# Kernel tuning notes

Measured on AMD Instinct MI355X. Metric: run time of the kernel, lower is better.

Reference implementation:

```python
import jax, jax.numpy as jnp
import numpy as np

N = 262144          # num keyframes
E = 1048576         # num visual links (edges)
DT = 0.1            # IMU integration step
L1, L2, L3, L4 = 1.0, 0.5, 2.0, 0.5
EPS = 1e-6

# ---- quaternion helpers (pypose convention: q = [x, y, z, w]) ----

def qmul(q1, q2):
    v1, w1 = q1[..., :3], q1[..., 3:4]
    v2, w2 = q2[..., :3], q2[..., 3:4]
    w = w1 * w2 - jnp.sum(v1 * v2, axis=-1, keepdims=True)
    v = w1 * v2 + w2 * v1 + jnp.cross(v1, v2)
    return jnp.concatenate([v, w], axis=-1)

def qconj(q):
    return jnp.concatenate([-q[..., :3], q[..., 3:4]], axis=-1)

def qrot(q, x):
    # rotate vector x by unit quaternion q: x + 2*cross(v, cross(v,x) + w*x)
    v, w = q[..., :3], q[..., 3:4]
    return x + 2.0 * jnp.cross(v, jnp.cross(v, x) + w * x)

def so3_log(q):
    # log map of unit quaternion -> axis-angle phi (..., 3)
    v, w = q[..., :3], q[..., 3:4]
    n = jnp.linalg.norm(v, axis=-1, keepdims=True)
    n_safe = jnp.where(n < EPS, 1.0, n)
    theta = 2.0 * jnp.arctan2(n, w)
    w_safe = jnp.where(jnp.abs(w) < EPS, 1.0, w)
    factor = jnp.where(n < EPS, 2.0 / w_safe, theta / n_safe)
    return factor * v

def se3_inv(p):
    t, q = p[..., :3], p[..., 3:]
    qi = qconj(q)
    ti = -qrot(qi, t)
    return jnp.concatenate([ti, qi], axis=-1)

def se3_mul(p1, p2):
    t1, q1 = p1[..., :3], p1[..., 3:]
    t2, q2 = p2[..., :3], p2[..., 3:]
    t = t1 + qrot(q1, t2)
    return jnp.concatenate([t, qmul(q1, q2)], axis=-1)

def se3_log(p):
    # returns se(3) tensor [tau, phi] (pypose order) with tau = Jl^{-1}(phi) t
    t, q = p[..., :3], p[..., 3:]
    phi = so3_log(q)
    th = jnp.linalg.norm(phi, axis=-1, keepdims=True)
    th_safe = jnp.where(th < EPS, 1.0, th)
    coef = jnp.where(
        th < EPS,
        1.0 / 12.0 + th * th / 720.0,
        1.0 / (th_safe * th_safe)
        - (1.0 + jnp.cos(th_safe)) / (2.0 * th_safe * jnp.sin(th_safe)),
    )
    pxt = jnp.cross(phi, t)
    tau = t - 0.5 * pxt + coef * jnp.cross(phi, pxt)
    return jnp.concatenate([tau, phi], axis=-1)


def setup_inputs() -> dict:
    key = jax.random.key(0)
    ks = jax.random.split(key, 8)

    def unit_quat(k, n):
        q = jax.random.normal(k, (n, 4), dtype=jnp.float32)
        return q / jnp.linalg.norm(q, axis=-1, keepdims=True)

    pose = jnp.concatenate(
        [jax.random.normal(ks[0], (N, 3), dtype=jnp.float32),
         unit_quat(ks[1], N)], axis=-1)
    vel = jax.random.normal(ks[2], (N, 3), dtype=jnp.float32)
    vmot = jnp.concatenate(
        [0.1 * jax.random.normal(ks[3], (E, 3), dtype=jnp.float32),
         unit_quat(ks[4], E)], axis=-1)
    imu_drot = unit_quat(ks[5], N - 1)
    body_dvel = 0.1 * jax.random.normal(ks[6], (N - 1, 3), dtype=jnp.float32)
    body_dpos = 0.1 * jax.random.normal(ks[7], (N - 1, 3), dtype=jnp.float32)
    vlink = jax.random.randint(jax.random.fold_in(key, 99), (E, 2), 0, N)
    return dict(pose=pose, vel=vel, vmot=vmot, imu_drot=imu_drot,
                body_dvel=body_dvel, body_dpos=body_dpos, vlink=vlink)


def reference(pose, vel, vmot, imu_drot, body_dvel, body_dpos, vlink):
    trans, rot = pose[:, :3], pose[:, 3:]
    r1 = rot[:-1]

    # IMU model: world-frame increments (rotation-dependent, as in original)
    imu_dvel = qrot(r1, body_dvel)                      # world_dvel(pose.rotation())
    imu_dpos = qrot(r1, body_dpos) + vel[:-1] * DT      # world_dpos(rot, vel)

    # pose-graph residual: Log(vmot^{-1} @ pose1^{-1} @ pose2)  [E, 6]
    pose1 = pose[vlink[:, 0]]
    pose2 = pose[vlink[:, 1]]
    err = se3_mul(se3_inv(vmot), se3_mul(se3_inv(pose1), pose2))
    pgerr = se3_log(err)

    # adjacent velocity residual [N-1, 3]
    adjvelerr = imu_dvel - jnp.diff(vel, axis=0)

    # IMU rotation residual: Log(imu_drot @ R1^{-1} @ R2)  [N-1, 3]
    q_rel = qmul(imu_drot, qmul(qconj(rot[:-1]), rot[1:]))
    imuroterr = so3_log(q_rel)

    # translation/velocity residual [N-1, 3]
    transvelerr = imu_dpos - jnp.diff(trans, axis=0)

    return jnp.concatenate([
        L1 * pgerr.reshape(-1),
        L2 * adjvelerr.reshape(-1),
        L3 * imuroterr.reshape(-1),
        L4 * transvelerr.reshape(-1),
    ], axis=0)
```

## Files before the change

kernel.cpp:

```cpp
#include <hip/hip_runtime.h>
#include <math.h>

constexpr int   NN  = 262144;
constexpr int   NE  = 1048576;
constexpr int   NE2 = NE / 2;
constexpr float DTc = 0.1f;
constexpr float W1 = 1.0f, W2 = 0.5f, W3 = 2.0f, W4 = 0.5f;
constexpr float EPSc = 1e-6f;

typedef float    __attribute__((ext_vector_type(2))) f32x2;
typedef float    __attribute__((ext_vector_type(4))) f32x4;
typedef float    __attribute__((ext_vector_type(4), aligned(4))) f32x4u;
typedef float    __attribute__((ext_vector_type(2), aligned(4))) f32x2u;
typedef int      __attribute__((ext_vector_type(2))) i32x2;
typedef _Float16 __attribute__((ext_vector_type(8))) f16x8;

struct V3 { float x, y, z; };
struct Q4 { float x, y, z, w; };

__device__ __forceinline__ V3 v3(float x, float y, float z) { V3 r{x, y, z}; return r; }
__device__ __forceinline__ V3 vadd(V3 a, V3 b) { return v3(a.x + b.x, a.y + b.y, a.z + b.z); }
__device__ __forceinline__ V3 vsub(V3 a, V3 b) { return v3(a.x - b.x, a.y - b.y, a.z - b.z); }
__device__ __forceinline__ V3 vscale(float s, V3 a) { return v3(s * a.x, s * a.y, s * a.z); }
__device__ __forceinline__ V3 vcross(V3 a, V3 b) {
    return v3(a.y * b.z - a.z * b.y, a.z * b.x - a.x * b.z, a.x * b.y - a.y * b.x);
}
__device__ __forceinline__ float vdot(V3 a, V3 b) { return a.x * b.x + a.y * b.y + a.z * b.z; }

__device__ __forceinline__ Q4 qmul(Q4 a, Q4 b) {
    Q4 r;
    r.w = a.w * b.w - (a.x * b.x + a.y * b.y + a.z * b.z);
    r.x = a.w * b.x + b.w * a.x + (a.y * b.z - a.z * b.y);
    r.y = a.w * b.y + b.w * a.y + (a.z * b.x - a.x * b.z);
    r.z = a.w * b.z + b.w * a.z + (a.x * b.y - a.y * b.x);
    return r;
}
__device__ __forceinline__ Q4 qconj(Q4 q) { Q4 r{-q.x, -q.y, -q.z, q.w}; return r; }
__device__ __forceinline__ V3 qrot(Q4 q, V3 x) {
    V3 v = v3(q.x, q.y, q.z);
    V3 c1 = vadd(vcross(v, x), vscale(q.w, x));
    return vadd(x, vscale(2.0f, vcross(v, c1)));
}
__device__ __forceinline__ V3 so3_log(Q4 q) {
    V3 v = v3(q.x, q.y, q.z);
    float n = sqrtf(vdot(v, v));
    float theta = 2.0f * atan2f(n, q.w);
    float factor;
    if (n < EPSc) {
        float w_safe = (fabsf(q.w) < EPSc) ? 1.0f : q.w;
        factor = 2.0f / w_safe;
    } else {
        factor = theta / n;
    }
    return vscale(factor, v);
}

__device__ __forceinline__ void edge_residual(V3 tm, Q4 qm, V3 t1, Q4 q1,
                                              V3 t2, Q4 q2, float* __restrict__ o) {
    Q4 qa = qconj(q1);
    V3 ta = vscale(-1.0f, qrot(qa, t1));
    V3 tb = vadd(ta, qrot(qa, t2));
    Q4 qb = qmul(qa, q2);
    Q4 qc = qconj(qm);
    V3 tc = vscale(-1.0f, qrot(qc, tm));
    V3 te = vadd(tc, qrot(qc, tb));
    Q4 qe = qmul(qc, qb);

    V3 phi = so3_log(qe);
    float th = sqrtf(vdot(phi, phi));
    float coef;
    if (th < EPSc) {
        coef = 1.0f / 12.0f + th * th / 720.0f;
    } else {
        float s, c;
        sincosf(th, &s, &c);
        coef = 1.0f / (th * th) - (1.0f + c) / (2.0f * th * s);
    }
    V3 pxt = vcross(phi, te);
    V3 tau = vadd(vsub(te, vscale(0.5f, pxt)), vscale(coef, vcross(phi, pxt)));

    f32x2* o2 = (f32x2*)o;
    f32x2 a = {W1 * tau.x, W1 * tau.y};
    f32x2 b = {W1 * tau.z, W1 * phi.x};
    f32x2 c = {W1 * phi.y, W1 * phi.z};
    __builtin_nontemporal_store(a, o2);
    __builtin_nontemporal_store(b, o2 + 1);
    __builtin_nontemporal_store(c, o2 + 2);
}

__global__ __launch_bounds__(256) void node_pack_kernel(
    const float* __restrict__ pose, const float* __restrict__ vel,
    const float* __restrict__ imu_drot, const float* __restrict__ body_dvel,
    const float* __restrict__ body_dpos, f16x8* __restrict__ ppH,
    float* __restrict__ out)
{
    int i = blockIdx.x * blockDim.x + threadIdx.x;
    if (i >= NN) return;
    f32x4u pa0 = *(const f32x4u*)(pose + 7 * (size_t)i);
    f32x4u pa1 = *(const f32x4u*)(pose + 7 * (size_t)i + 3);
    f16x8 rec = {(_Float16)pa0.x, (_Float16)pa0.y, (_Float16)pa0.z,
                 (_Float16)pa1.x, (_Float16)pa1.y, (_Float16)pa1.z,
                 (_Float16)pa1.w, (_Float16)0.0f};
    ppH[i] = rec;
    if (i >= NN - 1) return;

    V3 tr1 = v3(pa0.x, pa0.y, pa0.z); Q4 r1 = {pa1.x, pa1.y, pa1.z, pa1.w};
    f32x4u pb0 = *(const f32x4u*)(pose + 7 * (size_t)(i + 1));
    f32x4u pb1 = *(const f32x4u*)(pose + 7 * (size_t)(i + 1) + 3);
    V3 tr2 = v3(pb0.x, pb0.y, pb0.z); Q4 r2 = {pb1.x, pb1.y, pb1.z, pb1.w};

    f32x4u vv = *(const f32x4u*)(vel + 3 * (size_t)i);
    f32x2u vw = *(const f32x2u*)(vel + 3 * (size_t)i + 4);
    V3 v1 = v3(vv.x, vv.y, vv.z);
    V3 v2 = v3(vv.w, vw.x, vw.y);
    f32x2u bv0 = *(const f32x2u*)(body_dvel + 3 * (size_t)i);
    float  bv2 = body_dvel[3 * (size_t)i + 2];
    f32x2u bp0 = *(const f32x2u*)(body_dpos + 3 * (size_t)i);
    float  bp2 = body_dpos[3 * (size_t)i + 2];
    V3 bdv = v3(bv0.x, bv0.y, bv2);
    V3 bdp = v3(bp0.x, bp0.y, bp2);
    f32x4 id4 = *(const f32x4*)(imu_drot + 4 * (size_t)i);
    Q4 idr = {id4.x, id4.y, id4.z, id4.w};

    V3 imu_dvel = qrot(r1, bdv);
    V3 adjvel = vsub(imu_dvel, vsub(v2, v1));
    Q4 qrel = qmul(idr, qmul(qconj(r1), r2));
    V3 imurot = so3_log(qrel);
    V3 imu_dpos = vadd(qrot(r1, bdp), vscale(DTc, v1));
    V3 transvel = vsub(imu_dpos, vsub(tr2, tr1));

    size_t base = (size_t)6 * NE;
    size_t nm1 = (size_t)(NN - 1);
    float* oa = out + base + 3 * (size_t)i;
    oa[0] = W2 * adjvel.x; oa[1] = W2 * adjvel.y; oa[2] = W2 * adjvel.z;
    float* ob = out + base + 3 * nm1 + 3 * (size_t)i;
    ob[0] = W3 * imurot.x; ob[1] = W3 * imurot.y; ob[2] = W3 * imurot.z;
    float* oc = out + base + 6 * nm1 + 3 * (size_t)i;
    oc[0] = W4 * transvel.x; oc[1] = W4 * transvel.y; oc[2] = W4 * transvel.z;
}

__global__ __launch_bounds__(256) void edge_kernel(
    const float* __restrict__ vmot, const int* __restrict__ vlink,
    const f16x8* __restrict__ ppH, float* __restrict__ out)
{
    int tid = blockIdx.x * blockDim.x + threadIdx.x;
    if (tid >= NE2) return;
    int e0 = tid, e1 = tid + NE2;

    i32x2 l0 = __builtin_nontemporal_load((const i32x2*)vlink + e0);
    i32x2 l1 = __builtin_nontemporal_load((const i32x2*)vlink + e1);
    f32x4u m0a = __builtin_nontemporal_load((const f32x4u*)(vmot + 7 * (size_t)e0));
    f32x4u m0b = __builtin_nontemporal_load((const f32x4u*)(vmot + 7 * (size_t)e0 + 3));
    f32x4u m1a = __builtin_nontemporal_load((const f32x4u*)(vmot + 7 * (size_t)e1));
    f32x4u m1b = __builtin_nontemporal_load((const f32x4u*)(vmot + 7 * (size_t)e1 + 3));
    f16x8 g10 = ppH[l0.x];
    f16x8 g20 = ppH[l0.y];
    f16x8 g11 = ppH[l1.x];
    f16x8 g21 = ppH[l1.y];

    edge_residual(v3(m0a.x, m0a.y, m0a.z), Q4{m0b.x, m0b.y, m0b.z, m0b.w},
                  v3((float)g10[0], (float)g10[1], (float)g10[2]),
                  Q4{(float)g10[3], (float)g10[4], (float)g10[5], (float)g10[6]},
                  v3((float)g20[0], (float)g20[1], (float)g20[2]),
                  Q4{(float)g20[3], (float)g20[4], (float)g20[5], (float)g20[6]},
                  out + 6 * (size_t)e0);
    edge_residual(v3(m1a.x, m1a.y, m1a.z), Q4{m1b.x, m1b.y, m1b.z, m1b.w},
                  v3((float)g11[0], (float)g11[1], (float)g11[2]),
                  Q4{(float)g11[3], (float)g11[4], (float)g11[5], (float)g11[6]},
                  v3((float)g21[0], (float)g21[1], (float)g21[2]),
                  Q4{(float)g21[3], (float)g21[4], (float)g21[5], (float)g21[6]},
                  out + 6 * (size_t)e1);
}

__global__ __launch_bounds__(256) void vigraph_fallback(
    const float* __restrict__ pose, const float* __restrict__ vel,
    const float* __restrict__ vmot, const float* __restrict__ imu_drot,
    const float* __restrict__ body_dvel, const float* __restrict__ body_dpos,
    const int* __restrict__ vlink, float* __restrict__ out)
{
    int tid = blockIdx.x * blockDim.x + threadIdx.x;
    if (tid < NE) {
        int e = tid;
        const float* pm = vmot + 7 * (size_t)e;
        int i1 = vlink[2 * (size_t)e];
        int i2 = vlink[2 * (size_t)e + 1];
        const float* p1 = pose + 7 * (size_t)i1;
        const float* p2 = pose + 7 * (size_t)i2;
        edge_residual(v3(pm[0], pm[1], pm[2]), Q4{pm[3], pm[4], pm[5], pm[6]},
                      v3(p1[0], p1[1], p1[2]), Q4{p1[3], p1[4], p1[5], p1[6]},
                      v3(p2[0], p2[1], p2[2]), Q4{p2[3], p2[4], p2[5], p2[6]},
                      out + 6 * (size_t)e);
    } else {
        int i = tid - NE;
        if (i >= NN - 1) return;
        const float* pa = pose + 7 * (size_t)i;
        const float* pb = pose + 7 * (size_t)(i + 1);
        V3 tr1 = v3(pa[0], pa[1], pa[2]); Q4 r1 = {pa[3], pa[4], pa[5], pa[6]};
        V3 tr2 = v3(pb[0], pb[1], pb[2]); Q4 r2 = {pb[3], pb[4], pb[5], pb[6]};
        V3 v1 = v3(vel[3 * (size_t)i], vel[3 * (size_t)i + 1], vel[3 * (size_t)i + 2]);
        V3 v2 = v3(vel[3 * (size_t)(i + 1)], vel[3 * (size_t)(i + 1) + 1], vel[3 * (size_t)(i + 1) + 2]);
        V3 bdv = v3(body_dvel[3 * (size_t)i], body_dvel[3 * (size_t)i + 1], body_dvel[3 * (size_t)i + 2]);
        V3 bdp = v3(body_dpos[3 * (size_t)i], body_dpos[3 * (size_t)i + 1], body_dpos[3 * (size_t)i + 2]);
        Q4 idr = {imu_drot[4 * (size_t)i], imu_drot[4 * (size_t)i + 1],
                  imu_drot[4 * (size_t)i + 2], imu_drot[4 * (size_t)i + 3]};
        V3 imu_dvel = qrot(r1, bdv);
        V3 adjvel = vsub(imu_dvel, vsub(v2, v1));
        Q4 qrel = qmul(idr, qmul(qconj(r1), r2));
        V3 imurot = so3_log(qrel);
        V3 imu_dpos = vadd(qrot(r1, bdp), vscale(DTc, v1));
        V3 transvel = vsub(imu_dpos, vsub(tr2, tr1));
        size_t base = (size_t)6 * NE;
        size_t nm1 = (size_t)(NN - 1);
        float* oa = out + base + 3 * (size_t)i;
        oa[0] = W2 * adjvel.x; oa[1] = W2 * adjvel.y; oa[2] = W2 * adjvel.z;
        float* ob = out + base + 3 * nm1 + 3 * (size_t)i;
        ob[0] = W3 * imurot.x; ob[1] = W3 * imurot.y; ob[2] = W3 * imurot.z;
        float* oc = out + base + 6 * nm1 + 3 * (size_t)i;
        oc[0] = W4 * transvel.x; oc[1] = W4 * transvel.y; oc[2] = W4 * transvel.z;
    }
}

extern "C" void kernel_launch(void* const* d_in, const int* in_sizes, int n_in,
                              void* d_out, int out_size, void* d_ws, size_t ws_size,
                              hipStream_t stream) {
    const float* pose      = (const float*)d_in[0];
    const float* vel       = (const float*)d_in[1];
    const float* vmot      = (const float*)d_in[2];
    const float* imu_drot  = (const float*)d_in[3];
    const float* body_dvel = (const float*)d_in[4];
    const float* body_dpos = (const float*)d_in[5];
    const int*   vlink     = (const int*)d_in[6];
    float* out = (float*)d_out;

    const size_t table_bytes = (size_t)NN * 16;
    if (ws_size >= table_bytes) {
        f16x8* ppH = (f16x8*)d_ws;
        node_pack_kernel<<<NN / 256, 256, 0, stream>>>(pose, vel, imu_drot,
                                                       body_dvel, body_dpos, ppH, out);
        edge_kernel<<<NE2 / 256, 256, 0, stream>>>(vmot, vlink, ppH, out);
    } else {
        int total = NE + (NN - 1);
        int grid = (total + 255) / 256;
        vigraph_fallback<<<grid, 256, 0, stream>>>(pose, vel, vmot, imu_drot,
                                                   body_dvel, body_dpos, vlink, out);
    }
}
```

Measured before the change: 40.23 us.

## Process adjacent edge pairs per thread with wide loads and split node kernel

Each edge thread now handles two consecutive edges instead of edges e and e+NE/2, so vlink is read as one 16-byte load, vmot as contiguous 56 bytes, and the 12 outputs go out as three 16-byte nontemporal stores. The node pack is split into a light pack kernel that runs before the edge kernel, and the IMU residual work moves to a separate kernel launched after it. The SE3 algebra is also simplified to rotate t2-t1 and tb-tm once each instead of rotating twice. The split adds a third kernel launch and puts the pose read in two separate kernels.

New measurement: 42.73 us. 1.06x slower.

```diff
diff --git a/kernel.cpp b/kernel.cpp
--- a/kernel.cpp
+++ b/kernel.cpp
@@ -3,7 +3,7 @@
 
 constexpr int   NN  = 262144;
 constexpr int   NE  = 1048576;
-constexpr int   NE2 = NE / 2;
+constexpr int   NEP = NE / 2;
 constexpr float DTc = 0.1f;
 constexpr float W1 = 1.0f, W2 = 0.5f, W3 = 2.0f, W4 = 0.5f;
 constexpr float EPSc = 1e-6f;
@@ -12,7 +12,7 @@
 typedef float    __attribute__((ext_vector_type(4))) f32x4;
 typedef float    __attribute__((ext_vector_type(4), aligned(4))) f32x4u;
 typedef float    __attribute__((ext_vector_type(2), aligned(4))) f32x2u;
-typedef int      __attribute__((ext_vector_type(2))) i32x2;
+typedef int      __attribute__((ext_vector_type(4))) i32x4;
 typedef _Float16 __attribute__((ext_vector_type(8))) f16x8;
 
 struct V3 { float x, y, z; };
@@ -55,15 +55,15 @@
     return vscale(factor, v);
 }
 
-__device__ __forceinline__ void edge_residual(V3 tm, Q4 qm, V3 t1, Q4 q1,
-                                              V3 t2, Q4 q2, float* __restrict__ o) {
+struct TP { V3 tau; V3 phi; };
+
+__device__ __forceinline__ TP edge_residual(V3 tm, Q4 qm, V3 t1, Q4 q1,
+                                            V3 t2, Q4 q2) {
     Q4 qa = qconj(q1);
-    V3 ta = vscale(-1.0f, qrot(qa, t1));
-    V3 tb = vadd(ta, qrot(qa, t2));
+    V3 tb = qrot(qa, vsub(t2, t1));
     Q4 qb = qmul(qa, q2);
     Q4 qc = qconj(qm);
-    V3 tc = vscale(-1.0f, qrot(qc, tm));
-    V3 te = vadd(tc, qrot(qc, tb));
+    V3 te = qrot(qc, vsub(tb, tm));
     Q4 qe = qmul(qc, qb);
 
     V3 phi = so3_log(qe);
@@ -78,32 +78,70 @@
     }
     V3 pxt = vcross(phi, te);
     V3 tau = vadd(vsub(te, vscale(0.5f, pxt)), vscale(coef, vcross(phi, pxt)));
-
-    f32x2* o2 = (f32x2*)o;
-    f32x2 a = {W1 * tau.x, W1 * tau.y};
-    f32x2 b = {W1 * tau.z, W1 * phi.x};
-    f32x2 c = {W1 * phi.y, W1 * phi.z};
-    __builtin_nontemporal_store(a, o2);
-    __builtin_nontemporal_store(b, o2 + 1);
-    __builtin_nontemporal_store(c, o2 + 2);
-}
-
-__global__ __launch_bounds__(256) void node_pack_kernel(
+    TP r; r.tau = tau; r.phi = phi; return r;
+}
+
+__global__ __launch_bounds__(256) void pack_kernel(const float* __restrict__ pose,
+                                                   f16x8* __restrict__ ppH) {
+    int i = blockIdx.x * blockDim.x + threadIdx.x;
+    if (i >= NN) return;
+    f32x4u a = *(const f32x4u*)(pose + 7 * (size_t)i);
+    f32x4u b = *(const f32x4u*)(pose + 7 * (size_t)i + 3);
+    f16x8 rec = {(_Float16)a.x, (_Float16)a.y, (_Float16)a.z,
+                 (_Float16)b.x, (_Float16)b.y, (_Float16)b.z,
+                 (_Float16)b.w, (_Float16)0.0f};
+    ppH[i] = rec;
+}
+
+__global__ __launch_bounds__(256) void edge_kernel(
+    const float* __restrict__ vmot, const int* __restrict__ vlink,
+    const f16x8* __restrict__ ppH, float* __restrict__ out)
+{
+    int t = blockIdx.x * blockDim.x + threadIdx.x;
+    if (t >= NEP) return;
+
+    i32x4 l = __builtin_nontemporal_load((const i32x4*)vlink + t);
+    f16x8 g10 = ppH[l.x];
+    f16x8 g20 = ppH[l.y];
+    f16x8 g11 = ppH[l.z];
+    f16x8 g21 = ppH[l.w];
+    const float* pm = vmot + 14 * (size_t)t;
+    f32x4u ma = *(const f32x4u*)(pm);
+    f32x4u mb = *(const f32x4u*)(pm + 4);
+    f32x4u mc = *(const f32x4u*)(pm + 8);
+    f32x2u md = *(const f32x2u*)(pm + 12);
+
+    TP r0 = edge_residual(
+        v3(ma.x, ma.y, ma.z), Q4{ma.w, mb.x, mb.y, mb.z},
+        v3((float)g10[0], (float)g10[1], (float)g10[2]),
+        Q4{(float)g10[3], (float)g10[4], (float)g10[5], (float)g10[6]},
+        v3((float)g20[0], (float)g20[1], (float)g20[2]),
+        Q4{(float)g20[3], (float)g20[4], (float)g20[5], (float)g20[6]});
+    TP r1 = edge_residual(
+        v3(mb.w, mc.x, mc.y), Q4{mc.z, mc.w, md.x, md.y},
+        v3((float)g11[0], (float)g11[1], (float)g11[2]),
+        Q4{(float)g11[3], (float)g11[4], (float)g11[5], (float)g11[6]},
+        v3((float)g21[0], (float)g21[1], (float)g21[2]),
+        Q4{(float)g21[3], (float)g21[4], (float)g21[5], (float)g21[6]});
+
+    f32x4* o4 = (f32x4*)(out + 12 * (size_t)t);
+    f32x4 s0 = {W1 * r0.tau.x, W1 * r0.tau.y, W1 * r0.tau.z, W1 * r0.phi.x};
+    f32x4 s1 = {W1 * r0.phi.y, W1 * r0.phi.z, W1 * r1.tau.x, W1 * r1.tau.y};
+    f32x4 s2 = {W1 * r1.tau.z, W1 * r1.phi.x, W1 * r1.phi.y, W1 * r1.phi.z};
+    __builtin_nontemporal_store(s0, o4);
+    __builtin_nontemporal_store(s1, o4 + 1);
+    __builtin_nontemporal_store(s2, o4 + 2);
+}
+
+__global__ __launch_bounds__(256) void node_kernel(
     const float* __restrict__ pose, const float* __restrict__ vel,
     const float* __restrict__ imu_drot, const float* __restrict__ body_dvel,
-    const float* __restrict__ body_dpos, f16x8* __restrict__ ppH,
-    float* __restrict__ out)
+    const float* __restrict__ body_dpos, float* __restrict__ out)
 {
     int i = blockIdx.x * blockDim.x + threadIdx.x;
-    if (i >= NN) return;
+    if (i >= NN - 1) return;
     f32x4u pa0 = *(const f32x4u*)(pose + 7 * (size_t)i);
     f32x4u pa1 = *(const f32x4u*)(pose + 7 * (size_t)i + 3);
-    f16x8 rec = {(_Float16)pa0.x, (_Float16)pa0.y, (_Float16)pa0.z,
-                 (_Float16)pa1.x, (_Float16)pa1.y, (_Float16)pa1.z,
-                 (_Float16)pa1.w, (_Float16)0.0f};
-    ppH[i] = rec;
-    if (i >= NN - 1) return;
-
     V3 tr1 = v3(pa0.x, pa0.y, pa0.z); Q4 r1 = {pa1.x, pa1.y, pa1.z, pa1.w};
     f32x4u pb0 = *(const f32x4u*)(pose + 7 * (size_t)(i + 1));
     f32x4u pb1 = *(const f32x4u*)(pose + 7 * (size_t)(i + 1) + 3);
@@ -137,39 +175,6 @@
     ob[0] = W3 * imurot.x; ob[1] = W3 * imurot.y; ob[2] = W3 * imurot.z;
     float* oc = out + base + 6 * nm1 + 3 * (size_t)i;
     oc[0] = W4 * transvel.x; oc[1] = W4 * transvel.y; oc[2] = W4 * transvel.z;
-}
-
-__global__ __launch_bounds__(256) void edge_kernel(
-    const float* __restrict__ vmot, const int* __restrict__ vlink,
-    const f16x8* __restrict__ ppH, float* __restrict__ out)
-{
-    int tid = blockIdx.x * blockDim.x + threadIdx.x;
-    if (tid >= NE2) return;
-    int e0 = tid, e1 = tid + NE2;
-
-    i32x2 l0 = __builtin_nontemporal_load((const i32x2*)vlink + e0);
-    i32x2 l1 = __builtin_nontemporal_load((const i32x2*)vlink + e1);
-    f32x4u m0a = __builtin_nontemporal_load((const f32x4u*)(vmot + 7 * (size_t)e0));
-    f32x4u m0b = __builtin_nontemporal_load((const f32x4u*)(vmot + 7 * (size_t)e0 + 3));
-    f32x4u m1a = __builtin_nontemporal_load((const f32x4u*)(vmot + 7 * (size_t)e1));
-    f32x4u m1b = __builtin_nontemporal_load((const f32x4u*)(vmot + 7 * (size_t)e1 + 3));
-    f16x8 g10 = ppH[l0.x];
-    f16x8 g20 = ppH[l0.y];
-    f16x8 g11 = ppH[l1.x];
-    f16x8 g21 = ppH[l1.y];
-
-    edge_residual(v3(m0a.x, m0a.y, m0a.z), Q4{m0b.x, m0b.y, m0b.z, m0b.w},
-                  v3((float)g10[0], (float)g10[1], (float)g10[2]),
-                  Q4{(float)g10[3], (float)g10[4], (float)g10[5], (float)g10[6]},
-                  v3((float)g20[0], (float)g20[1], (float)g20[2]),
-                  Q4{(float)g20[3], (float)g20[4], (float)g20[5], (float)g20[6]},
-                  out + 6 * (size_t)e0);
-    edge_residual(v3(m1a.x, m1a.y, m1a.z), Q4{m1b.x, m1b.y, m1b.z, m1b.w},
-                  v3((float)g11[0], (float)g11[1], (float)g11[2]),
-                  Q4{(float)g11[3], (float)g11[4], (float)g11[5], (float)g11[6]},
-                  v3((float)g21[0], (float)g21[1], (float)g21[2]),
-                  Q4{(float)g21[3], (float)g21[4], (float)g21[5], (float)g21[6]},
-                  out + 6 * (size_t)e1);
 }
 
 __global__ __launch_bounds__(256) void vigraph_fallback(
@@ -186,10 +191,12 @@
         int i2 = vlink[2 * (size_t)e + 1];
         const float* p1 = pose + 7 * (size_t)i1;
         const float* p2 = pose + 7 * (size_t)i2;
-        edge_residual(v3(pm[0], pm[1], pm[2]), Q4{pm[3], pm[4], pm[5], pm[6]},
-                      v3(p1[0], p1[1], p1[2]), Q4{p1[3], p1[4], p1[5], p1[6]},
-                      v3(p2[0], p2[1], p2[2]), Q4{p2[3], p2[4], p2[5], p2[6]},
-                      out + 6 * (size_t)e);
+        TP r = edge_residual(v3(pm[0], pm[1], pm[2]), Q4{pm[3], pm[4], pm[5], pm[6]},
+                             v3(p1[0], p1[1], p1[2]), Q4{p1[3], p1[4], p1[5], p1[6]},
+                             v3(p2[0], p2[1], p2[2]), Q4{p2[3], p2[4], p2[5], p2[6]});
+        float* o = out + 6 * (size_t)e;
+        o[0] = W1 * r.tau.x; o[1] = W1 * r.tau.y; o[2] = W1 * r.tau.z;
+        o[3] = W1 * r.phi.x; o[4] = W1 * r.phi.y; o[5] = W1 * r.phi.z;
     } else {
         int i = tid - NE;
         if (i >= NN - 1) return;
@@ -235,9 +242,10 @@
     const size_t table_bytes = (size_t)NN * 16;
     if (ws_size >= table_bytes) {
         f16x8* ppH = (f16x8*)d_ws;
-        node_pack_kernel<<<NN / 256, 256, 0, stream>>>(pose, vel, imu_drot,
-                                                       body_dvel, body_dpos, ppH, out);
-        edge_kernel<<<NE2 / 256, 256, 0, stream>>>(vmot, vlink, ppH, out);
+        pack_kernel<<<NN / 256, 256, 0, stream>>>(pose, ppH);
+        edge_kernel<<<NEP / 256, 256, 0, stream>>>(vmot, vlink, ppH, out);
+        node_kernel<<<NN / 256, 256, 0, stream>>>(pose, vel, imu_drot,
+                                                  body_dvel, body_dpos, out);
     } else {
         int total = NE + (NN - 1);
         int grid = (total + 255) / 256;
```
